# Kernel optimization log

Hardware: AMD Instinct MI355X
Metric: run time of the kernel (lower is better)

Reference implementation:

```python
import jax, jax.numpy as jnp
import numpy as np

N = 100000      # nodes
E = 3200000     # edges (avg degree 32)
IN = 256        # in_channels
HID = 32        # hidden (hard-coded in module)
OUT = 40        # out_channels / classes
BN_EPS = 1e-5


def gcn_conv(x, W, b, src, dst, n):
    # PyG GCNConv: h = x @ W; add self-loops; symmetric norm D^-1/2 A D^-1/2; aggregate; + bias
    h = x @ W                                   # [n, d_out]
    loop = jnp.arange(n)
    s = jnp.concatenate([src, loop])            # [E+n]
    d = jnp.concatenate([dst, loop])
    deg = jax.ops.segment_sum(jnp.ones_like(d, dtype=h.dtype), d, num_segments=n)
    dinv = jnp.where(deg > 0, jax.lax.rsqrt(deg), 0.0)
    norm = dinv[s] * dinv[d]                    # [E+n]
    msg = h[s] * norm[:, None]                  # gather + scale
    return jax.ops.segment_sum(msg, d, num_segments=n) + b


def setup_inputs() -> dict:
    key = jax.random.key(0)
    k = jax.random.split(key, 4)
    x = jax.random.normal(k[0], (N, IN), dtype=jnp.float32)
    edge_index = jax.random.randint(k[1], (2, E), 0, N, dtype=jnp.int64)
    W1 = jax.random.normal(k[2], (IN, HID), dtype=jnp.float32) / np.float32(np.sqrt(IN))
    b1 = jnp.zeros((HID,), jnp.float32)
    W2 = jax.random.normal(k[3], (HID, OUT), dtype=jnp.float32) / np.float32(np.sqrt(HID))
    b2 = jnp.zeros((OUT,), jnp.float32)
    return {"x": x, "edge_index": edge_index, "W1": W1, "b1": b1, "W2": W2, "b2": b2}


def reference(x, edge_index, W1, b1, W2, b2):
    src, dst = edge_index[0], edge_index[1]
    h = jax.nn.elu(gcn_conv(x, W1, b1, src, dst, N))
    # BatchNorm1d created fresh each forward: batch stats, gamma=1, beta=0 (biased var)
    mean = jnp.mean(h, axis=0)
    var = jnp.mean((h - mean) ** 2, axis=0)
    h = (h - mean) * jax.lax.rsqrt(var + BN_EPS)
    h = jax.nn.relu(h)
    # Dropout(p=0.2): identity in eval / deterministic reference
    out = gcn_conv(h, W2, b2, src, dst, N)
    return jax.nn.log_softmax(out, axis=-1)
```

## Files before the change

### kernel.cpp

```cpp
#include <hip/hip_runtime.h>
#include <math.h>

typedef unsigned int uint;
typedef unsigned short ushort;
typedef float v2f __attribute__((ext_vector_type(2)));

__device__ __forceinline__ v2f fp8lo_to_f32(uint u) {
    return __builtin_amdgcn_cvt_pk_f32_fp8((int)u, false);
}
__device__ __forceinline__ v2f fp8hi_to_f32(uint u) {
    return __builtin_amdgcn_cvt_pk_f32_fp8((int)u, true);
}
__device__ __forceinline__ ushort f32x2_to_fp8(float a, float b) {
    return (ushort)(__builtin_amdgcn_cvt_pk_fp8_f32(a, b, 0, false) & 0xffff);
}

#define UNPACK8(r, f)                                                  \
    {                                                                  \
        v2f p0_ = fp8lo_to_f32((r).x), p1_ = fp8hi_to_f32((r).x);      \
        v2f p2_ = fp8lo_to_f32((r).y), p3_ = fp8hi_to_f32((r).y);      \
        f[0] += p0_.x; f[1] += p0_.y; f[2] += p1_.x; f[3] += p1_.y;    \
        f[4] += p2_.x; f[5] += p2_.y; f[6] += p3_.x; f[7] += p3_.y;    \
    }

#define NBU 49
#define NSEG 4
#define CELL 17408
#define SUBCAP 1280
#define CSRCAP 4608

__global__ __launch_bounds__(256) void k_bin(
    const int* __restrict__ src, const int* __restrict__ dst,
    int* __restrict__ cur, uint* __restrict__ ebuf, int E) {
    __shared__ int hist[NBU], base_[NBU], off[NBU];
    int tid = threadIdx.x;
    if (tid < NBU) { hist[tid] = 0; off[tid] = 0; }
    __syncthreads();
    int e0 = blockIdx.x * 4096 + tid;
    int s_[16], d_[16];
#pragma unroll
    for (int j = 0; j < 16; ++j) {
        int e = e0 + j * 256;
        if (e < E) {
            s_[j] = src[e]; d_[j] = dst[e];
            atomicAdd(&hist[d_[j] >> 11], 1);
        } else d_[j] = -1;
    }
    __syncthreads();
    int seg = blockIdx.x & 3;
    if (tid < NBU && hist[tid])
        base_[tid] = atomicAdd(&cur[tid * NSEG + seg], hist[tid]);
    __syncthreads();
#pragma unroll
    for (int j = 0; j < 16; ++j) {
        if (d_[j] >= 0) {
            int b = d_[j] >> 11;
            int p = base_[b] + atomicAdd(&off[b], 1);
            if (p < CELL)
                ebuf[(size_t)(b * NSEG + seg) * CELL + p] =
                    ((uint)(d_[j] & 2047) << 17) | (uint)s_[j];
        }
    }
}

__global__ __launch_bounds__(256) void k_bin2(
    const int* __restrict__ cur, const uint* __restrict__ ebuf,
    uint* __restrict__ subcell, int* __restrict__ slotlen) {
    __shared__ int curs[16], sbase[16];
    int tid = threadIdx.x;
    int b = blockIdx.x >> 2, seg = blockIdx.x & 3;
    if (tid < 16) {
        int sb = ((b * 16 + tid) * NSEG + seg) * SUBCAP;
        sbase[tid] = sb;
        curs[tid] = sb;
    }
    __syncthreads();
    int len = cur[b * NSEG + seg]; if (len > CELL) len = CELL;
    const uint* ep = ebuf + (size_t)(b * NSEG + seg) * CELL;
    int i = tid;
    for (; i + 768 < len; i += 1024) {
        uint v0 = ep[i], v1 = ep[i + 256], v2 = ep[i + 512], v3 = ep[i + 768];
        int u0 = (v0 >> 24) & 15, u1 = (v1 >> 24) & 15;
        int u2 = (v2 >> 24) & 15, u3 = (v3 >> 24) & 15;
        int p0 = atomicAdd(&curs[u0], 1);
        if (p0 - sbase[u0] < SUBCAP) subcell[p0] = v0;
        int p1 = atomicAdd(&curs[u1], 1);
        if (p1 - sbase[u1] < SUBCAP) subcell[p1] = v1;
        int p2 = atomicAdd(&curs[u2], 1);
        if (p2 - sbase[u2] < SUBCAP) subcell[p2] = v2;
        int p3 = atomicAdd(&curs[u3], 1);
        if (p3 - sbase[u3] < SUBCAP) subcell[p3] = v3;
    }
    for (; i < len; i += 256) {
        uint v = ep[i];
        int u = (v >> 24) & 15;
        int p = atomicAdd(&curs[u], 1);
        if (p - sbase[u] < SUBCAP) subcell[p] = v;
    }
    __syncthreads();
    if (tid < 16) {
        int c = curs[tid] - sbase[tid];
        slotlen[(b * 16 + tid) * NSEG + seg] = c < SUBCAP ? c : SUBCAP;
    }
}

__global__ __launch_bounds__(256) void k_sort3(
    const int* __restrict__ slotlen, const uint* __restrict__ subcell,
    uint* __restrict__ csr, int* __restrict__ rowstart, int* __restrict__ deg,
    float* __restrict__ dinv, int n) {
    __shared__ int hist[128];
    __shared__ int wtot;
    int tid = threadIdx.x;
    int bs = blockIdx.x;
    if (tid < 128) hist[tid] = 0;
    __syncthreads();
    int lens[NSEG];
    const uint* sp = subcell + (size_t)bs * NSEG * SUBCAP;
    for (int s = 0; s < NSEG; ++s) {
        int len = slotlen[bs * NSEG + s];
        lens[s] = len;
        const uint* ep = sp + s * SUBCAP;
        int i = tid;
        for (; i + 768 < len; i += 1024) {
            uint v0 = ep[i], v1 = ep[i + 256], v2 = ep[i + 512], v3 = ep[i + 768];
            atomicAdd(&hist[(v0 >> 17) & 127], 1);
            atomicAdd(&hist[(v1 >> 17) & 127], 1);
            atomicAdd(&hist[(v2 >> 17) & 127], 1);
            atomicAdd(&hist[(v3 >> 17) & 127], 1);
        }
        for (; i < len; i += 256) atomicAdd(&hist[(ep[i] >> 17) & 127], 1);
    }
    __syncthreads();
    int c = (tid < 128) ? hist[tid] : 0;
    int lane = tid & 63, w = tid >> 6;
    int incl = c;
#pragma unroll
    for (int o = 1; o < 64; o <<= 1) {
        int t = __shfl_up(incl, o, 64);
        if (lane >= o) incl += t;
    }
    if (w == 0 && lane == 63) wtot = incl;
    __syncthreads();
    int excl = incl - c + ((w == 1) ? wtot : 0);
    int csrBase = bs * CSRCAP;
    int node = bs * 128 + tid;
    if (tid < 128 && node < n) {
        deg[node] = c;
        dinv[node] = rsqrtf((float)c + 1.0f);
        rowstart[node] = csrBase + excl;
    }
    __syncthreads();
    if (tid < 128) hist[tid] = excl;
    __syncthreads();
    for (int s = 0; s < NSEG; ++s) {
        const uint* ep = sp + s * SUBCAP;
        int len = lens[s];
        int i = tid;
        for (; i + 768 < len; i += 1024) {
            uint v0 = ep[i], v1 = ep[i + 256], v2 = ep[i + 512], v3 = ep[i + 768];
            int p0 = atomicAdd(&hist[(v0 >> 17) & 127], 1);
            csr[csrBase + p0] = v0 & 0x1FFFFu;
            int p1 = atomicAdd(&hist[(v1 >> 17) & 127], 1);
            csr[csrBase + p1] = v1 & 0x1FFFFu;
            int p2 = atomicAdd(&hist[(v2 >> 17) & 127], 1);
            csr[csrBase + p2] = v2 & 0x1FFFFu;
            int p3 = atomicAdd(&hist[(v3 >> 17) & 127], 1);
            csr[csrBase + p3] = v3 & 0x1FFFFu;
        }
        for (; i < len; i += 256) {
            uint v = ep[i];
            int p = atomicAdd(&hist[(v >> 17) & 127], 1);
            csr[csrBase + p] = v & 0x1FFFFu;
        }
    }
}


__global__ __launch_bounds__(256) void k_gemm1(
    const float* __restrict__ x, const float* __restrict__ W,
    const float* __restrict__ dinv, ushort* __restrict__ h8, int n) {
    __shared__ float part[4 * 32 * 64];
    int lane = threadIdx.x & 63;
    int wv = __builtin_amdgcn_readfirstlane(threadIdx.x >> 6);
    int node0 = blockIdx.x * 64;
    int node = node0 + lane;
    int koff = wv * 64;

    float acc[32];
#pragma unroll
    for (int c = 0; c < 32; ++c) acc[c] = 0.f;
    if (node < n) {
        const float4* xr = (const float4*)(x + (size_t)node * 256 + koff);
#pragma unroll 4
        for (int j4 = 0; j4 < 16; ++j4) {
            float4 xv = xr[j4];
            const float* w0 = W + (koff + j4 * 4) * 32;
#pragma unroll
            for (int c = 0; c < 32; ++c) acc[c] += xv.x * w0[c];
#pragma unroll
            for (int c = 0; c < 32; ++c) acc[c] += xv.y * w0[32 + c];
#pragma unroll
            for (int c = 0; c < 32; ++c) acc[c] += xv.z * w0[64 + c];
#pragma unroll
            for (int c = 0; c < 32; ++c) acc[c] += xv.w * w0[96 + c];
        }
    }
    float* pw = part + wv * 2048 + lane;
#pragma unroll
    for (int c = 0; c < 32; ++c) pw[c * 64] = acc[c];
    __syncthreads();

    int rn = threadIdx.x >> 2;
    int cq = threadIdx.x & 3;
    int dnode = node0 + rn;
    if (dnode < n) {
        float di = dinv[dnode];
        ushort us[4];
#pragma unroll
        for (int half = 0; half < 4; ++half) {
            float v0 = 0.f, v1 = 0.f;
#pragma unroll
            for (int w = 0; w < 4; ++w) {
                v0 += part[w * 2048 + (cq * 8 + half * 2 + 0) * 64 + rn];
                v1 += part[w * 2048 + (cq * 8 + half * 2 + 1) * 64 + rn];
            }
            us[half] = f32x2_to_fp8(v0 * di, v1 * di);
        }
        uint2 p;
        p.x = (uint)us[0] | ((uint)us[1] << 16);
        p.y = (uint)us[2] | ((uint)us[3] << 16);
        *(uint2*)(h8 + (size_t)dnode * 16 + cq * 4) = p;
    }
}

__global__ __launch_bounds__(256) void k_agg1(
    const ushort* __restrict__ hs, const int* __restrict__ deg,
    const int* __restrict__ rowstart, const uint* __restrict__ csr,
    const float* __restrict__ dinv, const float* __restrict__ b1,
    ushort* __restrict__ y, float* __restrict__ partials, int n) {
    int tid = threadIdx.x;
    int l4 = tid & 3;
    int g  = tid >> 2;
    int d  = blockIdx.x * 64 + g;
    float sa[8], qa[8];
#pragma unroll
    for (int j = 0; j < 8; ++j) { sa[j] = 0.f; qa[j] = 0.f; }
    if (d < n) {
        float a[8], c[8];
#pragma unroll
        for (int j = 0; j < 8; ++j) { a[j] = 0.f; c[j] = 0.f; }
        uint2 sr = *((const uint2*)(hs + (size_t)d * 16) + l4);
        UNPACK8(sr, a);
        const uint* row = csr + rowstart[d];
        int end = deg[d];
        int k = 0;
        for (; k + 4 <= end; k += 4) {
            uint s0 = row[k], s1 = row[k+1], s2 = row[k+2], s3 = row[k+3];
            uint2 r0 = *((const uint2*)(hs + (size_t)s0 * 16) + l4);
            uint2 r1 = *((const uint2*)(hs + (size_t)s1 * 16) + l4);
            uint2 r2 = *((const uint2*)(hs + (size_t)s2 * 16) + l4);
            uint2 r3 = *((const uint2*)(hs + (size_t)s3 * 16) + l4);
            UNPACK8(r0, a); UNPACK8(r1, c);
            UNPACK8(r2, a); UNPACK8(r3, c);
        }
        for (; k < end; ++k) {
            uint2 r = *((const uint2*)(hs + (size_t)row[k] * 16) + l4);
            UNPACK8(r, a);
        }
        float di = dinv[d];
        float4 bA = *(const float4*)(b1 + l4 * 8);
        float4 bB = *(const float4*)(b1 + l4 * 8 + 4);
        float bv[8] = {bA.x, bA.y, bA.z, bA.w, bB.x, bB.y, bB.z, bB.w};
        float vv[8];
#pragma unroll
        for (int j = 0; j < 8; ++j) {
            float v = di * (a[j] + c[j]) + bv[j];
            v = v > 0.f ? v : expm1f(v);
            vv[j] = v; sa[j] = v; qa[j] = v * v;
        }
        ushort u0 = f32x2_to_fp8(vv[0], vv[1]);
        ushort u1 = f32x2_to_fp8(vv[2], vv[3]);
        ushort u2 = f32x2_to_fp8(vv[4], vv[5]);
        ushort u3 = f32x2_to_fp8(vv[6], vv[7]);
        uint2 pw;
        pw.x = (uint)u0 | ((uint)u1 << 16);
        pw.y = (uint)u2 | ((uint)u3 << 16);
        *((uint2*)(y + (size_t)d * 16) + l4) = pw;
    }
#pragma unroll
    for (int m = 4; m <= 32; m <<= 1) {
#pragma unroll
        for (int j = 0; j < 8; ++j) {
            sa[j] += __shfl_xor(sa[j], m, 64);
            qa[j] += __shfl_xor(qa[j], m, 64);
        }
    }
    __shared__ float wred[4][4][16];
    int lane = tid & 63, wv = tid >> 6;
    if (lane < 4) {
#pragma unroll
        for (int j = 0; j < 8; ++j) {
            wred[wv][lane][j]     = sa[j];
            wred[wv][lane][8 + j] = qa[j];
        }
    }
    __syncthreads();
    if (tid < 64) {
        int l4g = tid >> 4, slot = tid & 15;
        partials[(size_t)blockIdx.x * 64 + tid] =
            wred[0][l4g][slot] + wred[1][l4g][slot] +
            wred[2][l4g][slot] + wred[3][l4g][slot];
    }
}

__global__ __launch_bounds__(1024) void k_red(
    const float* __restrict__ partials, float* __restrict__ stats, int nblk) {
    __shared__ float red[1024];
    int t = threadIdx.x;
    int j = t & 63, w = t >> 6;
    float a = 0.f;
    for (int i = w; i < nblk; i += 16) a += partials[(size_t)i * 64 + j];
    red[t] = a;
    __syncthreads();
    if (t < 64) {
        float v = 0.f;
#pragma unroll
        for (int kk = 0; kk < 16; ++kk) v += red[kk * 64 + t];
        int l4g = t >> 4, slot = t & 15, c = l4g * 8 + (slot & 7);
        stats[(slot < 8) ? c : (32 + c)] = v;
    }
}

__global__ void k_bn2(const ushort* __restrict__ y, const float* __restrict__ stats,
                      const float* __restrict__ dinv, ushort* __restrict__ h2s, int n) {
    int t = blockIdx.x * blockDim.x + threadIdx.x;
    if (t >= n * 16) return;
    int i = t >> 4, c2 = (t & 15) * 2;
    float invn = 1.0f / (float)n;
    float m0 = stats[c2] * invn,    m1 = stats[c2+1] * invn;
    float v0 = stats[32+c2] * invn - m0*m0;
    float v1 = stats[33+c2] * invn - m1*m1;
    float s0 = rsqrtf(v0 + 1e-5f), s1 = rsqrtf(v1 + 1e-5f);
    float di = dinv[i];
    v2f u = fp8lo_to_f32(y[t]);
    float a = (u.x - m0) * s0; a = a > 0.f ? a : 0.f; a *= di;
    float b = (u.y - m1) * s1; b = b > 0.f ? b : 0.f; b *= di;
    h2s[t] = f32x2_to_fp8(a, b);
}

__global__ __launch_bounds__(256) void k_agg2(
    const ushort* __restrict__ h2s, const int* __restrict__ deg,
    const int* __restrict__ rowstart, const uint* __restrict__ csr,
    const float* __restrict__ dinv, const float* __restrict__ W2,
    const float* __restrict__ b2, float* __restrict__ out, int n) {
    __shared__ float w2s[1280];
    __shared__ float b2s[40];
    __shared__ float tb[64][33];
    int tid = threadIdx.x;
    for (int t = tid; t < 1280; t += 256) w2s[t] = W2[t];
    if (tid < 40) b2s[tid] = b2[tid];
    int l4 = tid & 3, g = tid >> 2;
    int d = blockIdx.x * 64 + g;
    if (d < n) {
        float a[8], c[8];
#pragma unroll
        for (int j = 0; j < 8; ++j) { a[j] = 0.f; c[j] = 0.f; }
        uint2 sr = *((const uint2*)(h2s + (size_t)d * 16) + l4);
        UNPACK8(sr, a);
        const uint* row = csr + rowstart[d];
        int end = deg[d];
        int k = 0;
        for (; k + 4 <= end; k += 4) {
            uint s0 = row[k], s1 = row[k+1], s2 = row[k+2], s3 = row[k+3];
            uint2 r0 = *((const uint2*)(h2s + (size_t)s0 * 16) + l4);
            uint2 r1 = *((const uint2*)(h2s + (size_t)s1 * 16) + l4);
            uint2 r2 = *((const uint2*)(h2s + (size_t)s2 * 16) + l4);
            uint2 r3 = *((const uint2*)(h2s + (size_t)s3 * 16) + l4);
            UNPACK8(r0, a); UNPACK8(r1, c);
            UNPACK8(r2, a); UNPACK8(r3, c);
        }
        for (; k < end; ++k) {
            uint2 r = *((const uint2*)(h2s + (size_t)row[k] * 16) + l4);
            UNPACK8(r, a);
        }
        float di = dinv[d];
#pragma unroll
        for (int j = 0; j < 8; ++j) tb[g][l4 * 8 + j] = di * (a[j] + c[j]);
    }
    __syncthreads();
    float o[10];
    const float* bp = b2s + l4 * 10;
#pragma unroll
    for (int m = 0; m < 10; ++m) o[m] = bp[m];
#pragma unroll
    for (int cc = 0; cc < 32; ++cc) {
        float tc = tb[g][cc];
        const float* wr = w2s + cc * 40 + l4 * 10;
#pragma unroll
        for (int m = 0; m < 10; ++m) o[m] += tc * wr[m];
    }
    float mx = o[0];
#pragma unroll
    for (int m = 1; m < 10; ++m) mx = fmaxf(mx, o[m]);
    mx = fmaxf(mx, __shfl_xor(mx, 1, 64));
    mx = fmaxf(mx, __shfl_xor(mx, 2, 64));
    float s = 0.f;
#pragma unroll
    for (int m = 0; m < 10; ++m) s += __expf(o[m] - mx);
    s += __shfl_xor(s, 1, 64);
    s += __shfl_xor(s, 2, 64);
    float lse = mx + __logf(s);
    if (d < n) {
        float* r = out + (size_t)d * 40 + l4 * 10;
#pragma unroll
        for (int m = 0; m < 10; m += 2) {
            float2 wv;
            wv.x = o[m] - lse; wv.y = o[m+1] - lse;
            *(float2*)(r + m) = wv;
        }
    }
}


extern "C" void kernel_launch(void* const* d_in, const int* in_sizes, int n_in,
                              void* d_out, int out_size, void* d_ws, size_t ws_size,
                              hipStream_t stream) {
    const float* x  = (const float*)d_in[0];
    const int*   ei = (const int*)d_in[1];
    const float* W1 = (const float*)d_in[2];
    const float* b1 = (const float*)d_in[3];
    const float* W2 = (const float*)d_in[4];
    const float* b2 = (const float*)d_in[5];

    int n = in_sizes[0] / 256;
    int E = in_sizes[1] / 2;
    const int* src = ei;
    const int* dst = ei + E;

    char*   base    = (char*)d_ws;
    ushort* hs8     = (ushort*)base;
    ushort* y       = (ushort*)(base + (size_t)n * 32);
    ushort* h2s     = (ushort*)(base + (size_t)n * 64);
    float*  dinv    = (float*) (base + (size_t)n * 96);
    int*    deg     = (int*)   (base + (size_t)n * 100);
    int*    rowstart= (int*)   (base + (size_t)n * 104);
    float*  stats   = (float*) (base + (size_t)n * 108);
    int*    cur     = (int*)   (base + (size_t)n * 108 + 256);
    int*    slotlen = (int*)   (base + (size_t)n * 108 + 1280);
    float*  partials= (float*) (base + (size_t)n * 108 + 13824);
    uint*   ebuf    = (uint*)  (base + (size_t)n * 108 + 538112);
    size_t  ebufB   = (size_t)NBU * NSEG * CELL * 4;
    uint*   subcell = (uint*)  ((char*)ebuf + ebufB);
    size_t  subB    = (size_t)NBU * 16 * NSEG * SUBCAP * 4;
    uint*   csr     = (uint*)  ((char*)subcell + subB);
    float*  out     = (float*)d_out;

    const int B = 256;
    int nb64 = (n + 63) / 64;

    hipMemsetAsync(cur, 0, NBU * NSEG * sizeof(int), stream);

    k_bin  <<<(E + 4095) / 4096, B, 0, stream>>>(src, dst, cur, ebuf, E);
    k_bin2 <<<NBU * NSEG, B, 0, stream>>>(cur, ebuf, subcell, slotlen);
    k_sort3<<<NBU * 16, B, 0, stream>>>(slotlen, subcell, csr, rowstart, deg,
                                        dinv, n);

    k_gemm1<<<(n + 63) / 64, B, 0, stream>>>(x, W1, dinv, hs8, n);
    k_agg1 <<<nb64, B, 0, stream>>>(hs8, deg, rowstart, csr, dinv, b1, y,
                                    partials, n);
    k_red  <<<1, 1024, 0, stream>>>(partials, stats, nb64);

    k_bn2<<<(n * 16 + B - 1) / B, B, 0, stream>>>(y, stats, dinv, h2s, n);

    k_agg2<<<nb64, B, 0, stream>>>(h2s, deg, rowstart, csr, dinv, W2, b2, out, n);
}
```

Measured before the change: 374.4 us.

## Stage x tile in LDS as bf16 and split GEMM1 by output columns

k_gemm1 now loads the 64x256 block of x cooperatively into swizzled shared memory, rounding each value to bf16. Each wavefront then computes 8 of the 32 output columns over the full K for its 64 nodes. This removes the cross-wave partial-sum reduction through shared memory and cuts the per-thread accumulator count from 32 to 8. In exchange it adds a bf16 rounding of the inputs, which costs precision, and every wave must read the whole K range from LDS.

```diff
diff --git a/kernel.cpp b/kernel.cpp
--- a/kernel.cpp
+++ b/kernel.cpp
@@ -179,57 +179,67 @@
 __global__ __launch_bounds__(256) void k_gemm1(
     const float* __restrict__ x, const float* __restrict__ W,
     const float* __restrict__ dinv, ushort* __restrict__ h8, int n) {
-    __shared__ float part[4 * 32 * 64];
-    int lane = threadIdx.x & 63;
-    int wv = __builtin_amdgcn_readfirstlane(threadIdx.x >> 6);
+    __shared__ ushort xl[64 * 256];
+    int tid = threadIdx.x;
     int node0 = blockIdx.x * 64;
+
+#pragma unroll 4
+    for (int i = 0; i < 16; ++i) {
+        int fidx = i * 1024 + tid * 4;
+        int row = fidx >> 8, k = fidx & 255;
+        uint bx = 0, by = 0;
+        if (node0 + row < n) {
+            float4 xv = *(const float4*)(x + (size_t)(node0 + row) * 256 + k);
+            uint r0 = (__float_as_uint(xv.x) + 0x8000u) >> 16;
+            uint r1 = (__float_as_uint(xv.y) + 0x8000u) >> 16;
+            uint r2 = (__float_as_uint(xv.z) + 0x8000u) >> 16;
+            uint r3 = (__float_as_uint(xv.w) + 0x8000u) >> 16;
+            bx = r0 | (r1 << 16); by = r2 | (r3 << 16);
+        }
+        int g = k >> 3;
+        int byteoff = row * 512 + (((g ^ (row & 31)) << 4) | ((k & 7) << 1));
+        *(uint2*)((char*)xl + byteoff) = make_uint2(bx, by);
+    }
+    __syncthreads();
+
+    int lane = tid & 63;
+    int wv = __builtin_amdgcn_readfirstlane(tid >> 6);
+    const char* xrow = (const char*)xl + lane * 512;
+    int rx = lane & 31;
+    const float* Wp = W + wv * 8;
+    float acc[8];
+#pragma unroll
+    for (int c = 0; c < 8; ++c) acc[c] = 0.f;
+#pragma unroll 2
+    for (int g = 0; g < 32; ++g) {
+        uint4 q = *(const uint4*)(xrow + (((g ^ rx) << 4)));
+        float xe[8];
+        xe[0] = __uint_as_float(q.x << 16);
+        xe[1] = __uint_as_float(q.x & 0xFFFF0000u);
+        xe[2] = __uint_as_float(q.y << 16);
+        xe[3] = __uint_as_float(q.y & 0xFFFF0000u);
+        xe[4] = __uint_as_float(q.z << 16);
+        xe[5] = __uint_as_float(q.z & 0xFFFF0000u);
+        xe[6] = __uint_as_float(q.w << 16);
+        xe[7] = __uint_as_float(q.w & 0xFFFF0000u);
+        const float* w0 = Wp + (size_t)(g * 8) * 32;
+#pragma unroll
+        for (int e = 0; e < 8; ++e) {
+#pragma unroll
+            for (int c = 0; c < 8; ++c) acc[c] += xe[e] * w0[e * 32 + c];
+        }
+    }
     int node = node0 + lane;
-    int koff = wv * 64;
-
-    float acc[32];
-#pragma unroll
-    for (int c = 0; c < 32; ++c) acc[c] = 0.f;
     if (node < n) {
-        const float4* xr = (const float4*)(x + (size_t)node * 256 + koff);
-#pragma unroll 4
-        for (int j4 = 0; j4 < 16; ++j4) {
-            float4 xv = xr[j4];
-            const float* w0 = W + (koff + j4 * 4) * 32;
-#pragma unroll
-            for (int c = 0; c < 32; ++c) acc[c] += xv.x * w0[c];
-#pragma unroll
-            for (int c = 0; c < 32; ++c) acc[c] += xv.y * w0[32 + c];
-#pragma unroll
-            for (int c = 0; c < 32; ++c) acc[c] += xv.z * w0[64 + c];
-#pragma unroll
-            for (int c = 0; c < 32; ++c) acc[c] += xv.w * w0[96 + c];
-        }
-    }
-    float* pw = part + wv * 2048 + lane;
-#pragma unroll
-    for (int c = 0; c < 32; ++c) pw[c * 64] = acc[c];
-    __syncthreads();
-
-    int rn = threadIdx.x >> 2;
-    int cq = threadIdx.x & 3;
-    int dnode = node0 + rn;
-    if (dnode < n) {
-        float di = dinv[dnode];
-        ushort us[4];
-#pragma unroll
-        for (int half = 0; half < 4; ++half) {
-            float v0 = 0.f, v1 = 0.f;
-#pragma unroll
-            for (int w = 0; w < 4; ++w) {
-                v0 += part[w * 2048 + (cq * 8 + half * 2 + 0) * 64 + rn];
-                v1 += part[w * 2048 + (cq * 8 + half * 2 + 1) * 64 + rn];
-            }
-            us[half] = f32x2_to_fp8(v0 * di, v1 * di);
-        }
+        float di = dinv[node];
+        ushort u0 = f32x2_to_fp8(acc[0] * di, acc[1] * di);
+        ushort u1 = f32x2_to_fp8(acc[2] * di, acc[3] * di);
+        ushort u2 = f32x2_to_fp8(acc[4] * di, acc[5] * di);
+        ushort u3 = f32x2_to_fp8(acc[6] * di, acc[7] * di);
         uint2 p;
-        p.x = (uint)us[0] | ((uint)us[1] << 16);
-        p.y = (uint)us[2] | ((uint)us[3] << 16);
-        *(uint2*)(h8 + (size_t)dnode * 16 + cq * 4) = p;
+        p.x = (uint)u0 | ((uint)u1 << 16);
+        p.y = (uint)u2 | ((uint)u3 << 16);
+        *((uint2*)(h8 + (size_t)node * 16) + wv) = p;
     }
 }
 
```

New measurement: 396.9 us. 1.06x slower.
